# Kernel tuning notes

Measured on AMD Instinct MI355X. Metric: run time of the kernel, lower is better.

The kernel has to match this reference:

```python
import jax, jax.numpy as jnp
import numpy as np

# Static architecture sizes (see shape_source)
B, H, W, NCH = 64, 64, 64, 3
K = 2                     # kernel at every stage
D = 20                    # bond_dim == virtual_dim
OUT = 10                  # output_dim
P1 = (H // K) * (W // K)          # 1024 patches, stage 1
P2 = P1 // (K * K)                # 256 patches, stage 2
P3 = P2 // (K * K)                # 64 patches, stage 3
FP = 2 * K * K                    # feature_dim per stage = 2*ker^2 = 8
FF = 2 * D                        # feature_dim of final MPS = 2*virtual_dim


def _unfold(x, k):
    # torch: x.unfold(2,k,k).unfold(3,k,k).reshape(b, k*k, -1, C)
    b, C, Hh, Ww = x.shape
    v = x.reshape(b, C, Hh // k, k, Ww // k, k).transpose(0, 1, 2, 4, 3, 5)
    return v.reshape(b, k * k, -1, C)   # [b, k^2, P, C] (raw reshape, faithful)


def _batchnorm(y, g, bb, eps=1e-5):
    # BatchNorm1d(C) on [b, C, L], training mode (batch stats), affine
    mu = jnp.mean(y, axis=(0, 2), keepdims=True)
    var = jnp.var(y, axis=(0, 2), keepdims=True)
    return g[None, :, None] * (y - mu) * jax.lax.rsqrt(var + eps) + bb[None, :, None]


def _mps(x, cores, label, alpha, omega):
    # Batched tensor-train contraction over independent per-patch MPS modules.
    # x:     [b, Fraw, P, S]  (S sites per MPS, P independent MPS modules)
    # cores: [P, S, 2*Fraw, D, D], label: [O, D, D], alpha/omega: [D]
    phi = jnp.concatenate([x, 1.0 - x], axis=1)              # [b, F, P, S]
    M = jnp.einsum('bfps,psfij->spbij', phi, cores)          # per-site transfer mats
    def step(c, m):
        return jnp.einsum('pbij,pbjk->pbik', c, m), None
    eye = jnp.broadcast_to(jnp.eye(cores.shape[-1], dtype=x.dtype), M.shape[1:])
    tot, _ = jax.lax.scan(step, eye, M)                      # [P, b, D, D]
    return jnp.einsum('i,pbij,ojk,k->bpo', alpha, tot, label, omega)  # [b, P, O]


def _cores(key, P, S, F):
    # near-identity init; sum_f phi_f = Fraw = F/2, so scale eye by 2/F
    return (jnp.eye(D, dtype=jnp.float32) * (2.0 / F)
            + 0.01 * jax.random.normal(key, (P, S, F, D, D), jnp.float32))


def setup_inputs() -> dict:
    ks = jax.random.split(jax.random.key(0), 12)
    one, zero = jnp.ones((D,), jnp.float32), jnp.zeros
    return {
        'x': jax.random.normal(ks[0], (B, NCH, H, W), jnp.float32),
        'cores1': _cores(ks[1], P1, NCH, FP),
        'label1': 0.1 * jax.random.normal(ks[2], (D, D, D), jnp.float32),
        'alpha1': one, 'omega1': one,
        'g1': jnp.ones((P1,), jnp.float32), 'b1': zero((P1,), jnp.float32),
        'cores2': _cores(ks[3], P2, D, FP),
        'label2': 0.1 * jax.random.normal(ks[4], (D, D, D), jnp.float32),
        'alpha2': one, 'omega2': one,
        'g2': jnp.ones((P2,), jnp.float32), 'b2': zero((P2,), jnp.float32),
        'cores3': _cores(ks[5], P3, D, FP),
        'label3': 0.1 * jax.random.normal(ks[6], (D, D, D), jnp.float32),
        'alpha3': one, 'omega3': one,
        'g3': jnp.ones((P3,), jnp.float32), 'b3': zero((P3,), jnp.float32),
        'coresF': _cores(ks[7], 1, P3, FF),
        'labelF': 0.1 * jax.random.normal(ks[8], (OUT, D, D), jnp.float32),
        'alphaF': one, 'omegaF': one,
    }


def reference(x, cores1, label1, alpha1, omega1, g1, b1,
              cores2, label2, alpha2, omega2, g2, b2,
              cores3, label3, alpha3, omega3, g3, b3,
              coresF, labelF, alphaF, omegaF):
    b = x.shape[0]
    u = _unfold(x, K)                              # [b, 4, P1, 3]
    y = _mps(u, cores1, label1, alpha1, omega1)    # [b, P1, D]
    y = _batchnorm(y, g1, b1).reshape(b, D, H // K, W // K)   # raw view, faithful
    u = _unfold(y, K)                              # [b, 4, P2, D]
    y = _mps(u, cores2, label2, alpha2, omega2)    # [b, P2, D]
    y = _batchnorm(y, g2, b2).reshape(b, D, H // (K * K), W // (K * K))
    u = _unfold(y, K)                              # [b, 4, P3, D]
    y = _mps(u, cores3, label3, alpha3, omega3)    # [b, P3, D]
    y = _batchnorm(y, g3, b3)
    y = jnp.transpose(y, (0, 2, 1))                # [b, D, P3]
    out = _mps(y[:, :, None, :], coresF, labelF, alphaF, omegaF)[:, 0, :]
    return out                                     # [b, OUT]
```

## Files before the change

### kernel.cpp

```cpp
#include <hip/hip_runtime.h>
#include <hip/hip_bf16.h>

typedef __attribute__((ext_vector_type(4))) float f32x4;
typedef __attribute__((ext_vector_type(8))) short s16x8;

static __device__ __forceinline__ short f2bf(float x) {
  __hip_bfloat16 h = __float2bfloat16(x);
  return *reinterpret_cast<short*>(&h);
}

static __device__ __forceinline__ void ldsbar() {
  asm volatile("s_waitcnt lgkmcnt(0)" ::: "memory");
  __builtin_amdgcn_s_barrier();
  asm volatile("" ::: "memory");
}

template<int STAGE>
__global__ __launch_bounds__(256)
void k_mps(const float* __restrict__ xsrc, const float* __restrict__ ysrc,
           const float* __restrict__ cores, const float* __restrict__ alpha,
           const float* __restrict__ label, const float* __restrict__ omega,
           const float* __restrict__ gam, const float* __restrict__ bet,
           float* __restrict__ yout) {
  constexpr int S = (STAGE == 1) ? 3 : 20;
  __shared__ __align__(16) float u4[S][64][4];
  __shared__ __align__(16) short Cl[2][32][168];
  __shared__ __align__(16) float vls[64][36];
  __shared__ float Lw_l[400];
  __shared__ float redA[4], redB[4], stats[2];

  const int p = blockIdx.x, t = threadIdx.x;
  const int b = t & 63, q = t >> 6;
  const int m = b & 15, quad = b >> 4;
  const int bl = q * 16 + m;

  const bool two = (t < 144);
  const float* cbase = cores + (size_t)p * S * 3200;

  float p0A[8], p0B[8], p1A[8], p1B[8];
#pragma unroll
  for (int g = 0; g < 8; ++g) p0A[g] = cbase[g * 400 + t];
  if (two) {
#pragma unroll
    for (int g = 0; g < 8; ++g) p0B[g] = cbase[g * 400 + 256 + t];
  }

  for (int e = t; e < 400; e += 256) {
    int o = e / 20, j = e % 20;
    float a = 0.f;
#pragma unroll
    for (int k = 0; k < 20; ++k) a = fmaf(label[o * 400 + j * 20 + k], omega[k], a);
    Lw_l[e] = a;
  }

  {
    int* cz = (int*)&Cl[0][0][0];
    for (int i = t; i < 5376; i += 256) cz[i] = 0;
    for (int i = t; i < 64 * 36; i += 256) {
      int col = i % 36;
      vls[i / 36][col] = (col < 20) ? alpha[col] : 0.f;
    }
  }

  for (int k = 0; k < S; ++k) {
    float val;
    if (STAGE == 1) {
      int L = q * 3072 + p * 3 + k;
      int c = L >> 12, r = L & 4095;
      int hh = 2 * (r >> 7) + ((r >> 1) & 1);
      int ww = 2 * ((r >> 2) & 31) + (r & 1);
      val = xsrc[(b * 3 + c) * 4096 + hh * 64 + ww];
    } else if (STAGE == 2) {
      int L = q * 5120 + p * 20 + k;
      int c = L >> 10, r = L & 1023;
      int f = c * 1024 + (2 * (r >> 6) + ((r >> 1) & 1)) * 32
                        + (2 * ((r >> 2) & 15) + (r & 1));
      val = ysrc[f * 64 + b];
    } else {
      int L = q * 1280 + p * 20 + k;
      int c = L >> 8, r = L & 255;
      int f = c * 256 + (2 * (r >> 5) + ((r >> 1) & 1)) * 16
                       + (2 * ((r >> 2) & 7) + (r & 1));
      val = ysrc[f * 64 + b];
    }
    u4[k][b][q] = val;
  }

  auto writeC = [&](int buf, int e, const float* r) {
    int i = e / 20, j = e % 20;
    Cl[buf][j][      i] = f2bf(r[0] - r[4]);
    Cl[buf][j][ 32 + i] = f2bf(r[1] - r[5]);
    Cl[buf][j][ 64 + i] = f2bf(r[2] - r[6]);
    Cl[buf][j][ 96 + i] = f2bf(r[3] - r[7]);
    float cs = r[4] + r[5] + r[6] + r[7];
    if (i == j) cs -= 1.f;
    Cl[buf][j][128 + i] = f2bf(cs);
  };
  auto loadSite = [&](int s, float (&rA)[8], float (&rB)[8]) {
    const float* cs = cbase + (size_t)s * 3200;
#pragma unroll
    for (int g = 0; g < 8; ++g) rA[g] = cs[g * 400 + t];
    if (two) {
#pragma unroll
      for (int g = 0; g < 8; ++g) rB[g] = cs[g * 400 + 256 + t];
    }
  };

  writeC(0, t, p0A);
  if (two) writeC(0, t + 256, p0B);
  if (S > 1) loadSite(1, p0A, p0B);
  if (S > 2) loadSite(2, p1A, p1B);
  ldsbar();

  auto site_step = [&](int s, int cur, float (&rA)[8], float (&rB)[8]) {
    const float4 uu = *(const float4*)&u4[s][bl][0];
    const float4 va = *(const float4*)&vls[bl][quad * 8];
    const float4 vb = *(const float4*)&vls[bl][quad * 8 + 4];
    const float vv[8] = {va.x, va.y, va.z, va.w, vb.x, vb.y, vb.z, vb.w};
    const float um[5] = {uu.x, uu.y, uu.z, uu.w, 1.f};

    if (s + 1 < S) {
      writeC(cur ^ 1, t, rA);
      if (two) writeC(cur ^ 1, t + 256, rB);
      if (s + 3 < S) loadSite(s + 3, rA, rB);
    }

    f32x4 acc0 = {0.f, 0.f, 0.f, 0.f};
    f32x4 acc1 = {0.f, 0.f, 0.f, 0.f};
#pragma unroll
    for (int kt = 0; kt < 5; ++kt) {
      s16x8 aF;
#pragma unroll
      for (int j2 = 0; j2 < 8; ++j2) aF[j2] = f2bf(vv[j2] * um[kt]);
      const s16x8 bF0 = *(const s16x8*)&Cl[cur][m][kt * 32 + quad * 8];
      const s16x8 bF1 = *(const s16x8*)&Cl[cur][m + 16][kt * 32 + quad * 8];
      acc0 = __builtin_amdgcn_mfma_f32_16x16x32_bf16(aF, bF0, acc0, 0, 0, 0);
      acc1 = __builtin_amdgcn_mfma_f32_16x16x32_bf16(aF, bF1, acc1, 0, 0, 0);
    }

#pragma unroll
    for (int r = 0; r < 4; ++r) vls[q * 16 + quad * 4 + r][m] += acc0[r];
    if (m < 4) {
#pragma unroll
      for (int r = 0; r < 4; ++r) vls[q * 16 + quad * 4 + r][m + 16] += acc1[r];
    }
    ldsbar();
  };

  for (int s = 0; s < S; s += 2) {
    site_step(s, 0, p0A, p0B);
    if (s + 1 < S) site_step(s + 1, 1, p1A, p1B);
  }

  float vf[20];
  {
    const float4 v0 = *(const float4*)&vls[b][0];
    const float4 v1 = *(const float4*)&vls[b][4];
    const float4 v2 = *(const float4*)&vls[b][8];
    const float4 v3 = *(const float4*)&vls[b][12];
    const float4 v4 = *(const float4*)&vls[b][16];
    vf[0]=v0.x; vf[1]=v0.y; vf[2]=v0.z; vf[3]=v0.w;
    vf[4]=v1.x; vf[5]=v1.y; vf[6]=v1.z; vf[7]=v1.w;
    vf[8]=v2.x; vf[9]=v2.y; vf[10]=v2.z; vf[11]=v2.w;
    vf[12]=v3.x; vf[13]=v3.y; vf[14]=v3.z; vf[15]=v3.w;
    vf[16]=v4.x; vf[17]=v4.y; vf[18]=v4.z; vf[19]=v4.w;
  }
  float yo[5];
  float s1 = 0.f, s2 = 0.f;
#pragma unroll
  for (int jj = 0; jj < 5; ++jj) {
    int o = q * 5 + jj;
    float a = 0.f;
#pragma unroll
    for (int j = 0; j < 20; ++j) a = fmaf(vf[j], Lw_l[o * 20 + j], a);
    yo[jj] = a; s1 += a; s2 += a * a;
  }
#pragma unroll
  for (int off = 32; off > 0; off >>= 1) {
    s1 += __shfl_down(s1, off); s2 += __shfl_down(s2, off);
  }
  if (b == 0) { redA[q] = s1; redB[q] = s2; }
  __syncthreads();
  if (t == 0) {
    float S1 = redA[0] + redA[1] + redA[2] + redA[3];
    float S2 = redB[0] + redB[1] + redB[2] + redB[3];
    float mu = S1 * (1.f / 1280.f);
    float var = S2 * (1.f / 1280.f) - mu * mu;
    if (var < 0.f) var = 0.f;
    stats[0] = mu; stats[1] = var;
  }
  __syncthreads();
  float mu = stats[0], var = stats[1];
  float scale = gam[p] / sqrtf(var + 1e-5f);
  float shift = bet[p] - mu * scale;
#pragma unroll
  for (int jj = 0; jj < 5; ++jj) {
    int o = q * 5 + jj;
    yout[(p * 20 + o) * 64 + b] = fmaf(yo[jj], scale, shift);
  }
}

__global__ __launch_bounds__(256)
void k_f1(const float* __restrict__ y3n, const float* __restrict__ coresF,
          float* __restrict__ PP) {
  const int bid = blockIdx.x;
  const int b = bid >> 3, c = bid & 7;
  const int t = threadIdx.x;
  __shared__ float ybuf[8][20];
  __shared__ float M[400];
  __shared__ float Pb[2][400];
  if (t < 160) ybuf[t / 20][t % 20] = y3n[(c * 160 + t) * 64 + b];
  __syncthreads();
  int cur = 0;
  for (int s = 0; s < 8; ++s) {
    const float* cf = coresF + (size_t)(c * 8 + s) * 16000;
    for (int e = t; e < 400; e += 256) {
      float m = 0.f;
#pragma unroll
      for (int g = 0; g < 20; ++g) {
        float lo = cf[g * 400 + e];
        float hi = cf[(g + 20) * 400 + e];
        m += fmaf(ybuf[s][g], lo - hi, hi);
      }
      M[e] = m;
    }
    __syncthreads();
    if (s == 0) {
      for (int e = t; e < 400; e += 256) Pb[0][e] = M[e];
    } else {
      for (int e = t; e < 400; e += 256) {
        int i = e / 20, j = e % 20;
        float a = 0.f;
#pragma unroll
        for (int k = 0; k < 20; ++k)
          a = fmaf(Pb[cur][i * 20 + k], M[k * 20 + j], a);
        Pb[cur ^ 1][e] = a;
      }
      cur ^= 1;
    }
    __syncthreads();
  }
  for (int e = t; e < 400; e += 256) PP[(size_t)bid * 400 + e] = Pb[cur][e];
}

__global__ __launch_bounds__(256)
void k_f2(const float* __restrict__ PP, const float* __restrict__ alphaF,
          const float* __restrict__ labelF, const float* __restrict__ omegaF,
          float* __restrict__ out) {
  const int b = blockIdx.x, t = threadIdx.x;
  __shared__ float Pb[2][400];
  __shared__ float M[400];
  __shared__ float va[20];
  __shared__ float LwF_l[200];
  if (t < 200) {
    int o = t / 20, j = t % 20;
    float a = 0.f;
#pragma unroll
    for (int k = 0; k < 20; ++k) a = fmaf(labelF[o * 400 + j * 20 + k], omegaF[k], a);
    LwF_l[t] = a;
  }
  for (int e = t; e < 400; e += 256) Pb[0][e] = PP[(size_t)b * 3200 + e];
  int cur = 0;
  for (int c = 1; c < 8; ++c) {
    for (int e = t; e < 400; e += 256) M[e] = PP[(size_t)b * 3200 + c * 400 + e];
    __syncthreads();
    for (int e = t; e < 400; e += 256) {
      int i = e / 20, j = e % 20;
      float a = 0.f;
#pragma unroll
      for (int k = 0; k < 20; ++k) a = fmaf(Pb[cur][i * 20 + k], M[k * 20 + j], a);
      Pb[cur ^ 1][e] = a;
    }
    cur ^= 1;
    __syncthreads();
  }
  if (t < 20) {
    float a = 0.f;
#pragma unroll
    for (int i = 0; i < 20; ++i) a = fmaf(alphaF[i], Pb[cur][i * 20 + t], a);
    va[t] = a;
  }
  __syncthreads();
  if (t < 10) {
    float a = 0.f;
#pragma unroll
    for (int j = 0; j < 20; ++j) a = fmaf(va[j], LwF_l[t * 20 + j], a);
    out[b * 10 + t] = a;
  }
}

extern "C" void kernel_launch(void* const* d_in, const int* in_sizes, int n_in,
                              void* d_out, int out_size, void* d_ws, size_t ws_size,
                              hipStream_t stream) {
  const float* x      = (const float*)d_in[0];
  const float* cores1 = (const float*)d_in[1];
  const float* label1 = (const float*)d_in[2];
  const float* alpha1 = (const float*)d_in[3];
  const float* omega1 = (const float*)d_in[4];
  const float* g1     = (const float*)d_in[5];
  const float* b1     = (const float*)d_in[6];
  const float* cores2 = (const float*)d_in[7];
  const float* label2 = (const float*)d_in[8];
  const float* alpha2 = (const float*)d_in[9];
  const float* omega2 = (const float*)d_in[10];
  const float* g2     = (const float*)d_in[11];
  const float* b2     = (const float*)d_in[12];
  const float* cores3 = (const float*)d_in[13];
  const float* label3 = (const float*)d_in[14];
  const float* alpha3 = (const float*)d_in[15];
  const float* omega3 = (const float*)d_in[16];
  const float* g3     = (const float*)d_in[17];
  const float* b3     = (const float*)d_in[18];
  const float* coresF = (const float*)d_in[19];
  const float* labelF = (const float*)d_in[20];
  const float* alphaF = (const float*)d_in[21];
  const float* omegaF = (const float*)d_in[22];

  float* ws  = (float*)d_ws;
  float* yn1 = ws;
  float* yn2 = yn1 + 1310720;
  float* yn3 = yn2 + 327680;
  float* PP  = yn3 + 81920;
  float* out = (float*)d_out;

  k_mps<1><<<1024, 256, 0, stream>>>(x, nullptr, cores1, alpha1, label1, omega1, g1, b1, yn1);
  k_mps<2><<<256, 256, 0, stream>>>(nullptr, yn1, cores2, alpha2, label2, omega2, g2, b2, yn2);
  k_mps<3><<<64, 256, 0, stream>>>(nullptr, yn2, cores3, alpha3, label3, omega3, g3, b3, yn3);
  k_f1<<<512, 256, 0, stream>>>(yn3, coresF, PP);
  k_f2<<<64, 256, 0, stream>>>(PP, alphaF, labelF, omegaF, out);
}
```

Before: 255.4 us.

## Fuse all MPS stages into one persistent kernel with grid barriers

```diff
diff --git a/kernel.cpp b/kernel.cpp
--- a/kernel.cpp
+++ b/kernel.cpp
@@ -15,21 +15,58 @@
   asm volatile("" ::: "memory");
 }
 
+__device__ __align__(128) unsigned g_cnt;
+__device__ __align__(128) unsigned g_gen;
+
+static __device__ __forceinline__ void gridbar(unsigned nb) {
+  __syncthreads();
+  if (threadIdx.x == 0) {
+    __threadfence();
+    unsigned gen = __hip_atomic_load(&g_gen, __ATOMIC_RELAXED, __HIP_MEMORY_SCOPE_AGENT);
+    unsigned arrived = __hip_atomic_fetch_add(&g_cnt, 1u, __ATOMIC_ACQ_REL,
+                                              __HIP_MEMORY_SCOPE_AGENT) + 1u;
+    if (arrived == nb) {
+      __hip_atomic_store(&g_cnt, 0u, __ATOMIC_RELAXED, __HIP_MEMORY_SCOPE_AGENT);
+      __hip_atomic_store(&g_gen, gen + 1u, __ATOMIC_RELEASE, __HIP_MEMORY_SCOPE_AGENT);
+    } else {
+      while (__hip_atomic_load(&g_gen, __ATOMIC_ACQUIRE, __HIP_MEMORY_SCOPE_AGENT) == gen)
+        __builtin_amdgcn_s_sleep(2);
+    }
+    __threadfence();
+  }
+  __syncthreads();
+}
+
+struct MpsSmem {
+  float u4[20][64][4];
+  short Cl[2][32][168];
+  float vls[64][36];
+  float Lw[400];
+  float redA[4], redB[4], stats[2];
+};
+struct F1Smem {
+  float ybuf[8][20];
+  float M[400];
+  float Pb[2][400];
+};
+struct F2Smem {
+  float Pb[2][400];
+  float M[400];
+  float va[20];
+  float LwF[200];
+};
+
 template<int STAGE>
-__global__ __launch_bounds__(256)
-void k_mps(const float* __restrict__ xsrc, const float* __restrict__ ysrc,
-           const float* __restrict__ cores, const float* __restrict__ alpha,
-           const float* __restrict__ label, const float* __restrict__ omega,
-           const float* __restrict__ gam, const float* __restrict__ bet,
-           float* __restrict__ yout) {
+static __device__ void mps_stage(MpsSmem& sm, int p, int t,
+    const float* __restrict__ xsrc, const float* __restrict__ ysrc,
+    const float* __restrict__ cores, const float* __restrict__ alpha,
+    const float* __restrict__ label, const float* __restrict__ omega,
+    const float* __restrict__ gam, const float* __restrict__ bet,
+    float* __restrict__ yout) {
   constexpr int S = (STAGE == 1) ? 3 : 20;
-  __shared__ __align__(16) float u4[S][64][4];
-  __shared__ __align__(16) short Cl[2][32][168];
-  __shared__ __align__(16) float vls[64][36];
-  __shared__ float Lw_l[400];
-  __shared__ float redA[4], redB[4], stats[2];
-
-  const int p = blockIdx.x, t = threadIdx.x;
+  auto& u4 = sm.u4; auto& Cl = sm.Cl; auto& vls = sm.vls;
+  auto& Lw_l = sm.Lw; auto& redA = sm.redA; auto& redB = sm.redB; auto& stats = sm.stats;
+
   const int b = t & 63, q = t >> 6;
   const int m = b & 15, quad = b >> 4;
   const int bl = q * 16 + m;
@@ -200,16 +237,12 @@
   }
 }
 
-__global__ __launch_bounds__(256)
-void k_f1(const float* __restrict__ y3n, const float* __restrict__ coresF,
-          float* __restrict__ PP) {
-  const int bid = blockIdx.x;
-  const int b = bid >> 3, c = bid & 7;
-  const int t = threadIdx.x;
-  __shared__ float ybuf[8][20];
-  __shared__ float M[400];
-  __shared__ float Pb[2][400];
-  if (t < 160) ybuf[t / 20][t % 20] = y3n[(c * 160 + t) * 64 + b];
+static __device__ void f1_body(F1Smem& sf, int bid2, int t,
+                               const float* __restrict__ y3n,
+                               const float* __restrict__ coresF,
+                               float* __restrict__ PP) {
+  const int b = bid2 >> 3, c = bid2 & 7;
+  if (t < 160) sf.ybuf[t / 20][t % 20] = y3n[(c * 160 + t) * 64 + b];
   __syncthreads();
   int cur = 0;
   for (int s = 0; s < 8; ++s) {
@@ -220,56 +253,53 @@
       for (int g = 0; g < 20; ++g) {
         float lo = cf[g * 400 + e];
         float hi = cf[(g + 20) * 400 + e];
-        m += fmaf(ybuf[s][g], lo - hi, hi);
+        m += fmaf(sf.ybuf[s][g], lo - hi, hi);
       }
-      M[e] = m;
+      sf.M[e] = m;
     }
     __syncthreads();
     if (s == 0) {
-      for (int e = t; e < 400; e += 256) Pb[0][e] = M[e];
+      for (int e = t; e < 400; e += 256) sf.Pb[0][e] = sf.M[e];
     } else {
       for (int e = t; e < 400; e += 256) {
         int i = e / 20, j = e % 20;
         float a = 0.f;
 #pragma unroll
         for (int k = 0; k < 20; ++k)
-          a = fmaf(Pb[cur][i * 20 + k], M[k * 20 + j], a);
-        Pb[cur ^ 1][e] = a;
+          a = fmaf(sf.Pb[cur][i * 20 + k], sf.M[k * 20 + j], a);
+        sf.Pb[cur ^ 1][e] = a;
       }
       cur ^= 1;
     }
     __syncthreads();
   }
-  for (int e = t; e < 400; e += 256) PP[(size_t)bid * 400 + e] = Pb[cur][e];
-}
-
-__global__ __launch_bounds__(256)
-void k_f2(const float* __restrict__ PP, const float* __restrict__ alphaF,
-          const float* __restrict__ labelF, const float* __restrict__ omegaF,
-          float* __restrict__ out) {
-  const int b = blockIdx.x, t = threadIdx.x;
-  __shared__ float Pb[2][400];
-  __shared__ float M[400];
-  __shared__ float va[20];
-  __shared__ float LwF_l[200];
+  for (int e = t; e < 400; e += 256) PP[(size_t)bid2 * 400 + e] = sf.Pb[cur][e];
+}
+
+static __device__ void f2_body(F2Smem& sf, int b, int t,
+                               const float* __restrict__ PP,
+                               const float* __restrict__ alphaF,
+                               const float* __restrict__ labelF,
+                               const float* __restrict__ omegaF,
+                               float* __restrict__ out) {
   if (t < 200) {
     int o = t / 20, j = t % 20;
     float a = 0.f;
 #pragma unroll
     for (int k = 0; k < 20; ++k) a = fmaf(labelF[o * 400 + j * 20 + k], omegaF[k], a);
-    LwF_l[t] = a;
-  }
-  for (int e = t; e < 400; e += 256) Pb[0][e] = PP[(size_t)b * 3200 + e];
+    sf.LwF[t] = a;
+  }
+  for (int e = t; e < 400; e += 256) sf.Pb[0][e] = PP[(size_t)b * 3200 + e];
   int cur = 0;
   for (int c = 1; c < 8; ++c) {
-    for (int e = t; e < 400; e += 256) M[e] = PP[(size_t)b * 3200 + c * 400 + e];
+    for (int e = t; e < 400; e += 256) sf.M[e] = PP[(size_t)b * 3200 + c * 400 + e];
     __syncthreads();
     for (int e = t; e < 400; e += 256) {
       int i = e / 20, j = e % 20;
       float a = 0.f;
 #pragma unroll
-      for (int k = 0; k < 20; ++k) a = fmaf(Pb[cur][i * 20 + k], M[k * 20 + j], a);
-      Pb[cur ^ 1][e] = a;
+      for (int k = 0; k < 20; ++k) a = fmaf(sf.Pb[cur][i * 20 + k], sf.M[k * 20 + j], a);
+      sf.Pb[cur ^ 1][e] = a;
     }
     cur ^= 1;
     __syncthreads();
@@ -277,16 +307,61 @@
   if (t < 20) {
     float a = 0.f;
 #pragma unroll
-    for (int i = 0; i < 20; ++i) a = fmaf(alphaF[i], Pb[cur][i * 20 + t], a);
-    va[t] = a;
+    for (int i = 0; i < 20; ++i) a = fmaf(alphaF[i], sf.Pb[cur][i * 20 + t], a);
+    sf.va[t] = a;
   }
   __syncthreads();
   if (t < 10) {
     float a = 0.f;
 #pragma unroll
-    for (int j = 0; j < 20; ++j) a = fmaf(va[j], LwF_l[t * 20 + j], a);
+    for (int j = 0; j < 20; ++j) a = fmaf(sf.va[j], sf.LwF[t * 20 + j], a);
     out[b * 10 + t] = a;
   }
+}
+
+__global__ __launch_bounds__(256, 2)
+void k_all(const float* __restrict__ x,
+           const float* __restrict__ cores1, const float* __restrict__ label1,
+           const float* __restrict__ alpha1, const float* __restrict__ omega1,
+           const float* __restrict__ g1, const float* __restrict__ b1,
+           const float* __restrict__ cores2, const float* __restrict__ label2,
+           const float* __restrict__ alpha2, const float* __restrict__ omega2,
+           const float* __restrict__ g2, const float* __restrict__ b2,
+           const float* __restrict__ cores3, const float* __restrict__ label3,
+           const float* __restrict__ alpha3, const float* __restrict__ omega3,
+           const float* __restrict__ g3, const float* __restrict__ b3,
+           const float* __restrict__ coresF, const float* __restrict__ labelF,
+           const float* __restrict__ alphaF, const float* __restrict__ omegaF,
+           float* __restrict__ yn1, float* __restrict__ yn2,
+           float* __restrict__ yn3, float* __restrict__ PP,
+           float* __restrict__ out) {
+  __shared__ __align__(16) char smem[sizeof(MpsSmem)];
+  MpsSmem& sm  = *reinterpret_cast<MpsSmem*>(smem);
+  F1Smem&  sf1 = *reinterpret_cast<F1Smem*>(smem);
+  F2Smem&  sf2 = *reinterpret_cast<F2Smem*>(smem);
+  const int bid = blockIdx.x, t = threadIdx.x;
+  constexpr unsigned NB = 256;
+
+  for (int i = 0; i < 4; ++i) {
+    mps_stage<1>(sm, bid * 4 + i, t, x, nullptr, cores1, alpha1, label1, omega1,
+                 g1, b1, yn1);
+    __syncthreads();
+  }
+  gridbar(NB);
+
+  mps_stage<2>(sm, bid, t, nullptr, yn1, cores2, alpha2, label2, omega2, g2, b2, yn2);
+  gridbar(NB);
+
+  if (bid < 64)
+    mps_stage<3>(sm, bid, t, nullptr, yn2, cores3, alpha3, label3, omega3, g3, b3, yn3);
+  gridbar(NB);
+
+  f1_body(sf1, bid, t, yn3, coresF, PP);
+  __syncthreads();
+  f1_body(sf1, bid + 256, t, yn3, coresF, PP);
+  gridbar(NB);
+
+  if (bid < 64) f2_body(sf2, bid, t, PP, alphaF, labelF, omegaF, out);
 }
 
 extern "C" void kernel_launch(void* const* d_in, const int* in_sizes, int n_in,
@@ -323,9 +398,10 @@
   float* PP  = yn3 + 81920;
   float* out = (float*)d_out;
 
-  k_mps<1><<<1024, 256, 0, stream>>>(x, nullptr, cores1, alpha1, label1, omega1, g1, b1, yn1);
-  k_mps<2><<<256, 256, 0, stream>>>(nullptr, yn1, cores2, alpha2, label2, omega2, g2, b2, yn2);
-  k_mps<3><<<64, 256, 0, stream>>>(nullptr, yn2, cores3, alpha3, label3, omega3, g3, b3, yn3);
-  k_f1<<<512, 256, 0, stream>>>(yn3, coresF, PP);
-  k_f2<<<64, 256, 0, stream>>>(PP, alphaF, labelF, omegaF, out);
-}
+  k_all<<<256, 256, 0, stream>>>(
+      x, cores1, label1, alpha1, omega1, g1, b1,
+      cores2, label2, alpha2, omega2, g2, b2,
+      cores3, label3, alpha3, omega3, g3, b3,
+      coresF, labelF, alphaF, omegaF,
+      yn1, yn2, yn3, PP, out);
+}
```

New measurement: 403.5 us. 1.58x slower.
